# Kernel optimization log

Measured on AMD Instinct MI355X. Metric: run time of the kernel, lower is better.

The kernel has to match this reference:

```python
import jax, jax.numpy as jnp
import numpy as np

DELTA = 1e-7
C = -0.5 * jnp.log(2.0 * jnp.pi)


def _softplus(v):
    return jax.nn.softplus(v) + DELTA


def _log_normal(v, mean=0.0, s=1.0, eps=1e-5):
    return -(v - mean) ** 2 / (2.0 * s ** 2 + eps) - jnp.log(s) + C


def _log_lognormal(v, mean=1.0, s=None, eps=1e-6):
    if s is None:
        s = _softplus(jnp.sqrt(jnp.log(2.0)))  # default prior scale
    return -(jnp.log(v) - mean) ** 2 / (2.0 * s ** 2 + eps) - jnp.log(v) - jnp.log(s) + C


def setup_inputs() -> dict:
    key = jax.random.key(0)
    ks = jax.random.split(key, 14)
    N, K, n_mc = 1024, 2, 64
    inp = {
        'x': jax.random.normal(ks[0], (N, K), dtype=jnp.float32),
        'y': jax.random.normal(ks[1], (N,), dtype=jnp.float32),
        'z': jax.random.normal(ks[2], (n_mc, 5), dtype=jnp.float32),
    }
    names = ['q_beta_m', 'q_beta_s', 'q_sigma2_m', 'q_sigma2_s', 'q_eta_m',
             'q_eta_s', 'q_ls_Z_m', 'q_ls_Z_s', 'q_ls_N_m', 'q_ls_N_s']
    for i, n in enumerate(names):
        inp[n] = jax.random.normal(ks[3 + i], (1,), dtype=jnp.float32)
    return inp


def reference(x, y, z, q_beta_m, q_beta_s, q_sigma2_m, q_sigma2_s,
              q_eta_m, q_eta_s, q_ls_Z_m, q_ls_Z_s, q_ls_N_m, q_ls_N_s):
    N = x.shape[0]
    # reparameterized samples (z plays the role of torch.randn(nMC, 5))
    sigma2 = jnp.exp(z[:, 0] * _softplus(q_sigma2_s) + q_sigma2_m)  # [M]
    beta = z[:, 1] * _softplus(q_beta_s) + q_beta_m                 # [M]
    eta = jnp.exp(z[:, 2] * _softplus(q_eta_s) + q_eta_m)          # [M]
    ls_Z = jnp.exp(z[:, 3] * _softplus(q_ls_Z_s) + q_ls_Z_m)
    ls_N = jnp.exp(z[:, 4] * _softplus(q_ls_N_s) + q_ls_N_m)
    ls = jnp.stack([ls_Z, ls_N], axis=1)                            # [M, 2]

    log_prior = (_log_normal(beta) + _log_lognormal(sigma2) + _log_lognormal(eta)
                 + _log_lognormal(ls[:, 0]) + _log_lognormal(ls[:, 1]))
    log_q = (_log_normal(beta, q_beta_m, _softplus(q_beta_s))
             + _log_lognormal(sigma2, q_sigma2_m, _softplus(q_sigma2_s))
             + _log_lognormal(eta, q_eta_m, _softplus(q_eta_s))
             + _log_lognormal(ls[:, 0], q_ls_Z_m, _softplus(q_ls_Z_s))
             + _log_lognormal(ls[:, 1], q_ls_N_m, _softplus(q_ls_N_s)))

    # RBF covariance per MC sample, built densely (diag of exp(-0.5*0)=1 matches W_ ones diag)
    x_ls = x[None, :, :] / ls[:, None, :]                           # [M, N, K]
    n2 = jnp.sum(x_ls ** 2, axis=-1)                                # [M, N]
    sqd = n2[:, :, None] + n2[:, None, :] - 2.0 * jnp.einsum('mik,mjk->mij', x_ls, x_ls)
    sqd = jnp.maximum(sqd, 0.0)
    cov = eta[:, None, None] * jnp.exp(-0.5 * sqd) + sigma2[:, None, None] * jnp.eye(N, dtype=x.dtype)

    # batched MVN log-prob via Cholesky
    L = jnp.linalg.cholesky(cov)                                    # [M, N, N]
    diff = y[None, :] - beta[:, None]                               # [M, N]
    sol = jax.scipy.linalg.solve_triangular(L, diff[..., None], lower=True)[..., 0]
    quad = jnp.sum(sol ** 2, axis=-1)
    logdet = 2.0 * jnp.sum(jnp.log(jnp.diagonal(L, axis1=-2, axis2=-1)), axis=-1)
    log_L = -0.5 * (quad + logdet + N * jnp.log(2.0 * jnp.pi))

    return log_L + log_prior - log_q
```

## Files before the change

kernel.cpp:

```cpp
#include <hip/hip_runtime.h>
#include <math.h>

#define NN 1024
#define NB 64
#define TB 128
#define CROSS (NN - TB)
#define NSAMP 64
#define SMPL 573440
#define TSQN (TB*TB)
#define PSQN (TB*512)

#define CCONST  (-0.91893853320467274f)
#define LOG2PI  (1.8378770664093453f)

__device__ __forceinline__ int rowoff(int i) {
    int b = i >> 6;
    return (2048*b + 3072)*b + (i & 63)*(64*b + 80);
}
__device__ __forceinline__ float bcastf(float v, int lane) {
    return __int_as_float(__builtin_amdgcn_readlane(__float_as_int(v), lane));
}
__device__ __forceinline__ float softplus_d(float v) {
    return (v > 20.f ? v : log1pf(expf(v))) + 1e-7f;
}
__device__ __forceinline__ float log_normal_f(float v, float mean, float s, float eps) {
    float d = v - mean;
    return -d * d / (2.f * s * s + eps) - logf(s) + CCONST;
}
__device__ __forceinline__ float log_lognormal_f(float v, float mean, float s) {
    float lv = logf(v);
    float d = lv - mean;
    return -d * d / (2.f * s * s + 1e-6f) - lv - logf(s) + CCONST;
}
__device__ __forceinline__ void fma4(float4& c, float a, const float4& b) {
    c.x = fmaf(a, b.x, c.x); c.y = fmaf(a, b.y, c.y);
    c.z = fmaf(a, b.z, c.z); c.w = fmaf(a, b.w, c.w);
}

__global__ void scal_kernel(const float* __restrict__ z,
    const float* qbm, const float* qbs, const float* qsm, const float* qss,
    const float* qem, const float* qes, const float* qzm, const float* qzs,
    const float* qnm, const float* qns, float* __restrict__ scal)
{
    int m = threadIdx.x;
    if (m >= NSAMP) return;
    float z0 = z[m*5+0], z1 = z[m*5+1], z2 = z[m*5+2], z3 = z[m*5+3], z4 = z[m*5+4];
    float spb = softplus_d(qbs[0]);
    float sps = softplus_d(qss[0]);
    float spe = softplus_d(qes[0]);
    float spz = softplus_d(qzs[0]);
    float spn = softplus_d(qns[0]);
    float sigma2 = expf(z0 * sps + qsm[0]);
    float beta   = z1 * spb + qbm[0];
    float eta    = expf(z2 * spe + qem[0]);
    float lsZ    = expf(z3 * spz + qzm[0]);
    float lsN    = expf(z4 * spn + qnm[0]);
    float s0 = softplus_d(sqrtf(logf(2.f)));
    float lp = log_normal_f(beta, 0.f, 1.f, 1e-5f)
             + log_lognormal_f(sigma2, 1.f, s0)
             + log_lognormal_f(eta,    1.f, s0)
             + log_lognormal_f(lsZ,    1.f, s0)
             + log_lognormal_f(lsN,    1.f, s0);
    float lq = log_normal_f(beta, qbm[0], spb, 1e-5f)
             + log_lognormal_f(sigma2, qsm[0], sps)
             + log_lognormal_f(eta,    qem[0], spe)
             + log_lognormal_f(lsZ,    qzm[0], spz)
             + log_lognormal_f(lsN,    qnm[0], spn);
    scal[m]           = sigma2;
    scal[NSAMP + m]   = eta;
    scal[2*NSAMP + m] = 1.f / lsZ;
    scal[3*NSAMP + m] = 1.f / lsN;
    scal[4*NSAMP + m] = beta;
    scal[5*NSAMP + m] = lp - lq;
}

__global__ __launch_bounds__(256)
void covslim_kernel(float* __restrict__ cov, float* __restrict__ tsq,
                    const float* __restrict__ scal,
                    const float* __restrict__ x, const float* __restrict__ y,
                    float* __restrict__ bvec, float* __restrict__ stats, int mbase)
{
    int ml = blockIdx.y;
    int m  = mbase + ml;
    float sigma2 = scal[m];
    float eta    = scal[NSAMP + m];
    float ilZ    = scal[2*NSAMP + m];
    float ilN    = scal[3*NSAMP + m];
    float* C = cov + (size_t)ml * SMPL;
    int tid = threadIdx.x;

    if (blockIdx.x == 0 && tid == 0) { stats[2*m] = 0.f; stats[2*m+1] = 0.f; }

    if (blockIdx.x < 64) {
        int i  = blockIdx.x * 16 + (tid >> 4);
        int j0 = (tid & 15) * 4;
        if ((tid & 15) == 0) bvec[(size_t)m * NN + i] = y[i] - scal[4*NSAMP + m];
        if (j0 > i) return;
        float xi0 = x[2*i]   * ilZ;
        float xi1 = x[2*i+1] * ilN;
        float4 xa = *(const float4*)(x + 2*j0);
        float4 xb = *(const float4*)(x + 2*j0 + 4);
        float v[4]; float d0, d1;
        d0 = xa.x*ilZ - xi0; d1 = xa.y*ilN - xi1; v[0] = eta*__expf(-0.5f*(d0*d0+d1*d1));
        d0 = xa.z*ilZ - xi0; d1 = xa.w*ilN - xi1; v[1] = eta*__expf(-0.5f*(d0*d0+d1*d1));
        d0 = xb.x*ilZ - xi0; d1 = xb.y*ilN - xi1; v[2] = eta*__expf(-0.5f*(d0*d0+d1*d1));
        d0 = xb.z*ilZ - xi0; d1 = xb.w*ilN - xi1; v[3] = eta*__expf(-0.5f*(d0*d0+d1*d1));
        #pragma unroll
        for (int q = 0; q < 4; ++q) if (j0 + q == i) v[q] += sigma2;
        float* row = C + rowoff(i);
        if (j0 + 3 <= i) {
            float4 o; o.x = v[0]; o.y = v[1]; o.z = v[2]; o.w = v[3];
            *(float4*)(row + j0) = o;
        } else {
            #pragma unroll
            for (int q = 0; q < 4; ++q) if (j0 + q <= i) row[j0+q] = v[q];
        }
    } else {
        int bx2 = blockIdx.x - 64;
        int tr  = bx2 * 8 + (tid >> 5);
        int tc  = (tid & 31) * 4;
        int i   = CROSS + tr;
        int j0  = CROSS + tc;
        float xi0 = x[2*i]   * ilZ;
        float xi1 = x[2*i+1] * ilN;
        float4 xa = *(const float4*)(x + 2*j0);
        float4 xb = *(const float4*)(x + 2*j0 + 4);
        float v[4]; float d0, d1;
        d0 = xa.x*ilZ - xi0; d1 = xa.y*ilN - xi1; v[0] = eta*__expf(-0.5f*(d0*d0+d1*d1));
        d0 = xa.z*ilZ - xi0; d1 = xa.w*ilN - xi1; v[1] = eta*__expf(-0.5f*(d0*d0+d1*d1));
        d0 = xb.x*ilZ - xi0; d1 = xb.y*ilN - xi1; v[2] = eta*__expf(-0.5f*(d0*d0+d1*d1));
        d0 = xb.z*ilZ - xi0; d1 = xb.w*ilN - xi1; v[3] = eta*__expf(-0.5f*(d0*d0+d1*d1));
        #pragma unroll
        for (int q = 0; q < 4; ++q) if (j0 + q == i) v[q] += sigma2;
        float4 o; o.x = v[0]; o.y = v[1]; o.z = v[2]; o.w = v[3];
        *(float4*)(tsq + (size_t)ml * TSQN + tr * TB + tc) = o;
    }
}

__global__ __launch_bounds__(256)
void update_kernel(float* __restrict__ covb, const float* __restrict__ scal,
                   const float* __restrict__ x, int mbase, int p, int mc)
{
    int bid = blockIdx.x;
    int ml  = bid % mc;
    int bx  = bid / mc;
    int m  = mbase + ml;
    float* C = covb + (size_t)ml * SMPL;
    int rowbase = p + bx * 128;
    int bofp = rowoff(p);
    int bsp  = 64*(p>>6) + 80;

    __shared__ __align__(16) float As[32][132];
    __shared__ __align__(16) float Bs[32][68];

    int tid = threadIdx.x;
    int tx = tid & 7,  ty = tid >> 3;
    int c0 = tx * 8,   r0 = ty * 4;

    float4 acc[4][2];
    #pragma unroll
    for (int r = 0; r < 4; ++r) { acc[r][0] = make_float4(0,0,0,0); acc[r][1] = make_float4(0,0,0,0); }

    float4 ra[4], rb[2];
    #pragma unroll
    for (int t = 0; t < 4; ++t) {
        int idx = tid + t * 256;
        int ii = idx >> 3, c4 = (idx & 7) << 2;
        int gr = rowbase + ii;
        ra[t] = make_float4(0,0,0,0);
        if (gr < NN) ra[t] = *(const float4*)(C + rowoff(gr) + c4);
    }
    #pragma unroll
    for (int t = 0; t < 2; ++t) {
        int idx = tid + t * 256;
        int ii = idx >> 3, c4 = (idx & 7) << 2;
        rb[t] = *(const float4*)(C + bofp + ii * bsp + c4);
    }

    for (int ks = 0; ks < p; ks += 32) {
        #pragma unroll
        for (int t = 0; t < 4; ++t) {
            int idx = tid + t * 256;
            int ii = idx >> 3, c4 = (idx & 7) << 2;
            As[c4+0][ii] = ra[t].x; As[c4+1][ii] = ra[t].y;
            As[c4+2][ii] = ra[t].z; As[c4+3][ii] = ra[t].w;
        }
        #pragma unroll
        for (int t = 0; t < 2; ++t) {
            int idx = tid + t * 256;
            int ii = idx >> 3, c4 = (idx & 7) << 2;
            Bs[c4+0][ii] = rb[t].x; Bs[c4+1][ii] = rb[t].y;
            Bs[c4+2][ii] = rb[t].z; Bs[c4+3][ii] = rb[t].w;
        }
        __syncthreads();
        int kn = ks + 32;
        if (kn < p) {
            #pragma unroll
            for (int t = 0; t < 4; ++t) {
                int idx = tid + t * 256;
                int ii = idx >> 3, c4 = (idx & 7) << 2;
                int gr = rowbase + ii;
                ra[t] = make_float4(0,0,0,0);
                if (gr < NN) ra[t] = *(const float4*)(C + rowoff(gr) + kn + c4);
            }
            #pragma unroll
            for (int t = 0; t < 2; ++t) {
                int idx = tid + t * 256;
                int ii = idx >> 3, c4 = (idx & 7) << 2;
                rb[t] = *(const float4*)(C + bofp + ii * bsp + kn + c4);
            }
        }
        #pragma unroll
        for (int k = 0; k < 32; ++k) {
            float4 b0 = *(const float4*)&Bs[k][c0];
            float4 b1 = *(const float4*)&Bs[k][c0 + 4];
            float4 a0 = *(const float4*)&As[k][r0];
            float ar[4] = {a0.x, a0.y, a0.z, a0.w};
            #pragma unroll
            for (int r = 0; r < 4; ++r) {
                fma4(acc[r][0], ar[r], b0);
                fma4(acc[r][1], ar[r], b1);
            }
        }
        __syncthreads();
    }

    int jcol = p + c0;
    float sigma2 = scal[m];
    float eta    = scal[NSAMP + m];
    float ilZ    = scal[2*NSAMP + m];
    float ilN    = scal[3*NSAMP + m];
    float4 xa0 = *(const float4*)(x + 2*jcol);
    float4 xb0 = *(const float4*)(x + 2*jcol + 4);
    float4 xa1 = *(const float4*)(x + 2*jcol + 8);
    float4 xb1 = *(const float4*)(x + 2*jcol + 12);
    #pragma unroll
    for (int r = 0; r < 4; ++r) {
        int g = rowbase + r0 + r;
        if (g < NN) {
            float xi0 = x[2*g]   * ilZ;
            float xi1 = x[2*g+1] * ilN;
            float v[8]; float d0, d1;
            d0 = xa0.x*ilZ - xi0; d1 = xa0.y*ilN - xi1; v[0] = eta*__expf(-0.5f*(d0*d0+d1*d1));
            d0 = xa0.z*ilZ - xi0; d1 = xa0.w*ilN - xi1; v[1] = eta*__expf(-0.5f*(d0*d0+d1*d1));
            d0 = xb0.x*ilZ - xi0; d1 = xb0.y*ilN - xi1; v[2] = eta*__expf(-0.5f*(d0*d0+d1*d1));
            d0 = xb0.z*ilZ - xi0; d1 = xb0.w*ilN - xi1; v[3] = eta*__expf(-0.5f*(d0*d0+d1*d1));
            d0 = xa1.x*ilZ - xi0; d1 = xa1.y*ilN - xi1; v[4] = eta*__expf(-0.5f*(d0*d0+d1*d1));
            d0 = xa1.z*ilZ - xi0; d1 = xa1.w*ilN - xi1; v[5] = eta*__expf(-0.5f*(d0*d0+d1*d1));
            d0 = xb1.x*ilZ - xi0; d1 = xb1.y*ilN - xi1; v[6] = eta*__expf(-0.5f*(d0*d0+d1*d1));
            d0 = xb1.z*ilZ - xi0; d1 = xb1.w*ilN - xi1; v[7] = eta*__expf(-0.5f*(d0*d0+d1*d1));
            #pragma unroll
            for (int qq = 0; qq < 8; ++qq) if (jcol + qq == g) v[qq] += sigma2;
            float* cp = C + rowoff(g) + jcol;
            float4 u0, u1;
            u0.x = v[0] - acc[r][0].x; u0.y = v[1] - acc[r][0].y;
            u0.z = v[2] - acc[r][0].z; u0.w = v[3] - acc[r][0].w;
            u1.x = v[4] - acc[r][1].x; u1.y = v[5] - acc[r][1].y;
            u1.z = v[6] - acc[r][1].z; u1.w = v[7] - acc[r][1].w;
            *(float4*)cp = u0;
            *((float4*)cp + 1) = u1;
        }
    }
}

__global__ __launch_bounds__(256)
void update_small_kernel(float* __restrict__ covb, const float* __restrict__ scal,
                         const float* __restrict__ x, int mbase, int p, int mc, int nbx)
{
    int bid  = blockIdx.x;
    int ml   = bid % mc;
    int rest = bid / mc;
    int bx   = rest % nbx;
    int zz   = rest / nbx;
    int m  = mbase + ml;
    float* C = covb + (size_t)ml * SMPL;
    int rowbase = p + bx * 64;
    int zoff = zz * 32;
    int bofp = rowoff(p);
    int bsp  = 64*(p>>6) + 80;

    __shared__ __align__(16) float As[32][68];
    __shared__ __align__(16) float Bs[32][36];

    int tid = threadIdx.x;
    int tx = tid & 7,  ty = tid >> 3;
    int c0 = tx * 4,   r0 = ty * 2;

    float4 acc0 = make_float4(0,0,0,0), acc1 = make_float4(0,0,0,0);

    float4 ra[2], rb1;
    #pragma unroll
    for (int t = 0; t < 2; ++t) {
        int idx = tid + t * 256;
        int ii = idx >> 3, c4 = (idx & 7) << 2;
        int gr = rowbase + ii;
        ra[t] = make_float4(0,0,0,0);
        if (gr < NN) ra[t] = *(const float4*)(C + rowoff(gr) + c4);
    }
    {
        int ii = tid >> 3, c4 = (tid & 7) << 2;
        rb1 = *(const float4*)(C + bofp + (zoff + ii) * bsp + c4);
    }

    for (int ks = 0; ks < p; ks += 32) {
        #pragma unroll
        for (int t = 0; t < 2; ++t) {
            int idx = tid + t * 256;
            int ii = idx >> 3, c4 = (idx & 7) << 2;
            As[c4+0][ii] = ra[t].x; As[c4+1][ii] = ra[t].y;
            As[c4+2][ii] = ra[t].z; As[c4+3][ii] = ra[t].w;
        }
        {
            int ii = tid >> 3, c4 = (tid & 7) << 2;
            Bs[c4+0][ii] = rb1.x; Bs[c4+1][ii] = rb1.y;
            Bs[c4+2][ii] = rb1.z; Bs[c4+3][ii] = rb1.w;
        }
        __syncthreads();
        int kn = ks + 32;
        if (kn < p) {
            #pragma unroll
            for (int t = 0; t < 2; ++t) {
                int idx = tid + t * 256;
                int ii = idx >> 3, c4 = (idx & 7) << 2;
                int gr = rowbase + ii;
                ra[t] = make_float4(0,0,0,0);
                if (gr < NN) ra[t] = *(const float4*)(C + rowoff(gr) + kn + c4);
            }
            {
                int ii = tid >> 3, c4 = (tid & 7) << 2;
                rb1 = *(const float4*)(C + bofp + (zoff + ii) * bsp + kn + c4);
            }
        }
        #pragma unroll
        for (int k = 0; k < 32; ++k) {
            float4 bv = *(const float4*)&Bs[k][c0];
            float2 av = *(const float2*)&As[k][r0];
            fma4(acc0, av.x, bv);
            fma4(acc1, av.y, bv);
        }
        __syncthreads();
    }

    int jcol = p + zoff + c0;
    float sigma2 = scal[m];
    float eta    = scal[NSAMP + m];
    float ilZ    = scal[2*NSAMP + m];
    float ilN    = scal[3*NSAMP + m];
    float4 xa = *(const float4*)(x + 2*jcol);
    float4 xb = *(const float4*)(x + 2*jcol + 4);
    int g0 = rowbase + r0;
    #pragma unroll
    for (int rr = 0; rr < 2; ++rr) {
        int g = g0 + rr;
        if (g < NN) {
            float xi0 = x[2*g]   * ilZ;
            float xi1 = x[2*g+1] * ilN;
            float v[4]; float d0, d1;
            d0 = xa.x*ilZ - xi0; d1 = xa.y*ilN - xi1; v[0] = eta*__expf(-0.5f*(d0*d0+d1*d1));
            d0 = xa.z*ilZ - xi0; d1 = xa.w*ilN - xi1; v[1] = eta*__expf(-0.5f*(d0*d0+d1*d1));
            d0 = xb.x*ilZ - xi0; d1 = xb.y*ilN - xi1; v[2] = eta*__expf(-0.5f*(d0*d0+d1*d1));
            d0 = xb.z*ilZ - xi0; d1 = xb.w*ilN - xi1; v[3] = eta*__expf(-0.5f*(d0*d0+d1*d1));
            #pragma unroll
            for (int qq = 0; qq < 4; ++qq) if (jcol + qq == g) v[qq] += sigma2;
            const float4 ac = (rr == 0) ? acc0 : acc1;
            float* cp = C + rowoff(g) + jcol;
            float4 u;
            u.x = v[0] - ac.x; u.y = v[1] - ac.y; u.z = v[2] - ac.z; u.w = v[3] - ac.w;
            *(float4*)cp = u;
        }
    }
}

__global__ __launch_bounds__(128)
void trsm_kernel(float* __restrict__ covb, float* __restrict__ bvec,
                 float* __restrict__ stats, int mbase, int p, int mc)
{
    int bid = blockIdx.x;
    int ml  = bid % mc;
    int bx  = bid / mc;
    int m  = mbase + ml;
    float* C = covb + (size_t)ml * SMPL;
    __shared__ __align__(16) float Tl[NB][68];
    __shared__ float rs_s[NB], sol_s[NB];
    int tid = threadIdx.x;
    int bofp = rowoff(p);
    int bsp  = 64*(p>>6) + 80;

    int r0 = p + NB + bx * 128 + tid;
    bool have = (r0 < NN);
    float l[NB];
    int roff = have ? rowoff(r0) : 0;
    if (have) {
        const float* rowp = C + roff + p;
        #pragma unroll
        for (int q = 0; q < NB/4; ++q) {
            float4 v = *(const float4*)(rowp + 4*q);
            l[4*q] = v.x; l[4*q+1] = v.y; l[4*q+2] = v.z; l[4*q+3] = v.w;
        }
    }

    if (tid < 64) {
        int r = tid;
        float row[NB];
        const float* src = C + bofp + r * bsp + p;
        #pragma unroll
        for (int q = 0; q < NB/4; ++q) {
            float4 v = *(const float4*)(src + 4*q);
            row[4*q+0] = v.x; row[4*q+1] = v.y; row[4*q+2] = v.z; row[4*q+3] = v.w;
        }
        float b = bvec[(size_t)m * NN + p + r];
        float quad_add = 0.f, my_d = 1.f, my_rs = 0.f, my_sol = 0.f;
        #pragma unroll
        for (int j = 0; j < NB; ++j) {
            float dj = fmaxf(bcastf(row[j], j), 1e-30f);
            float rs = rsqrtf(dj);
            if (r == j) my_d = dj;
            row[j] *= rs;
            float sj = bcastf(b, j) * rs;
            quad_add = fmaf(sj, sj, quad_add);
            b = fmaf(-row[j], sj, b);
            if (r == j) { my_rs = rs; my_sol = sj; }
            #pragma unroll
            for (int c = j + 1; c < NB; ++c) {
                float s = bcastf(row[j], c);
                row[c] = fmaf(-row[j], s, row[c]);
            }
        }
        #pragma unroll
        for (int q = 0; q < NB/4; ++q) {
            float4 v; v.x = row[4*q]; v.y = row[4*q+1]; v.z = row[4*q+2]; v.w = row[4*q+3];
            *(float4*)&Tl[r][4*q] = v;
        }
        rs_s[r]  = my_rs;
        sol_s[r] = my_sol;
        if (bx == 0) {
            float ldv = logf(my_d);
            #pragma unroll
            for (int off = 32; off > 0; off >>= 1) ldv += __shfl_down(ldv, off);
            if (r == 0) {
                stats[2*m]   += quad_add;
                stats[2*m+1] += ldv;
            }
        }
    }
    __syncthreads();

    if (!have) return;
    float* rowp = C + roff + p;
    #pragma unroll
    for (int j = 0; j < NB; ++j) {
        float s0 = l[j], s1 = 0.f, s2 = 0.f, s3 = 0.f;
        int c = 0;
        #pragma unroll
        for (; c + 4 <= j; c += 4) {
            float4 t = *(const float4*)&Tl[j][c];
            s0 = fmaf(-l[c],   t.x, s0);
            s1 = fmaf(-l[c+1], t.y, s1);
            s2 = fmaf(-l[c+2], t.z, s2);
            s3 = fmaf(-l[c+3], t.w, s3);
        }
        #pragma unroll
        for (; c < j; ++c) s0 = fmaf(-l[c], Tl[j][c], s0);
        l[j] = ((s0 + s1) + (s2 + s3)) * rs_s[j];
    }
    #pragma unroll
    for (int q = 0; q < NB/4; ++q) {
        float4 v; v.x = l[4*q]; v.y = l[4*q+1]; v.z = l[4*q+2]; v.w = l[4*q+3];
        *(float4*)(rowp + 4*q) = v;
    }
    float b0 = 0.f, b1 = 0.f, b2 = 0.f, b3 = 0.f;
    #pragma unroll
    for (int j = 0; j < NB; j += 4) {
        b0 = fmaf(l[j],   sol_s[j],   b0);
        b1 = fmaf(l[j+1], sol_s[j+1], b1);
        b2 = fmaf(l[j+2], sol_s[j+2], b2);
        b3 = fmaf(l[j+3], sol_s[j+3], b3);
    }
    bvec[(size_t)m * NN + r0] -= ((b0 + b1) + (b2 + b3));
}

__global__ __launch_bounds__(256)
void tailsyrk_kernel(const float* __restrict__ covb, float* __restrict__ psq)
{
    int ml = blockIdx.y;
    const float* C = covb + (size_t)ml * SMPL;
    float* P = psq + (size_t)ml * PSQN;
    int z  = blockIdx.x;
    int k0 = z * (CROSS / 4);

    __shared__ __align__(16) float As[32][132];
    int tid = threadIdx.x;
    int tx = tid & 15, ty = tid >> 4;
    int c0 = tx * 8, r0 = ty * 8;

    float4 acc[8][2];
    #pragma unroll
    for (int r = 0; r < 8; ++r) { acc[r][0] = make_float4(0,0,0,0); acc[r][1] = make_float4(0,0,0,0); }

    for (int ks = k0; ks < k0 + CROSS/4; ks += 32) {
        for (int idx = tid; idx < 128 * 8; idx += 256) {
            int ii = idx >> 3;
            int c4 = (idx & 7) << 2;
            float4 v = *(const float4*)(C + rowoff(CROSS + ii) + ks + c4);
            As[c4+0][ii] = v.x; As[c4+1][ii] = v.y;
            As[c4+2][ii] = v.z; As[c4+3][ii] = v.w;
        }
        __syncthreads();
        #pragma unroll
        for (int k = 0; k < 32; ++k) {
            float4 b0 = *(const float4*)&As[k][c0];
            float4 b1 = *(const float4*)&As[k][c0 + 4];
            float4 a0 = *(const float4*)&As[k][r0];
            float4 a1 = *(const float4*)&As[k][r0 + 4];
            float ar[8] = {a0.x, a0.y, a0.z, a0.w, a1.x, a1.y, a1.z, a1.w};
            #pragma unroll
            for (int r = 0; r < 8; ++r) {
                fma4(acc[r][0], ar[r], b0);
                fma4(acc[r][1], ar[r], b1);
            }
        }
        __syncthreads();
    }

    #pragma unroll
    for (int r = 0; r < 8; ++r) {
        float* cp = P + (r0 + r) * 512 + z * 128 + c0;
        *(float4*)cp = acc[r][0];
        *((float4*)cp + 1) = acc[r][1];
    }
}

__global__ __launch_bounds__(512)
void finish_kernel(const float* __restrict__ tsq, const float* __restrict__ psq,
                   const float* __restrict__ bvec,
                   const float* __restrict__ stats, float* __restrict__ out,
                   const float* __restrict__ scal, int mbase)
{
    int ml = blockIdx.x;
    int m  = mbase + ml;
    const float* T = tsq + (size_t)ml * TSQN;
    const float* P = psq + (size_t)ml * PSQN;
    __shared__ __align__(16) float A11[NB][68];
    __shared__ __align__(16) float A21[NB][68];
    __shared__ __align__(16) float A22[NB][68];
    __shared__ float rs_s[NB], sol_s[NB];
    __shared__ float bt[TB];
    __shared__ float s_quad, s_ld;
    int tid = threadIdx.x;

    if (tid < TB) bt[tid] = bvec[(size_t)m * NN + CROSS + tid];
    if (tid == 0) { s_quad = 0.f; s_ld = 0.f; }

    float4 tv[6], p0[6], p1[6], p2[6], p3[6];
    const float* pbase[6];
    #pragma unroll
    for (int u = 0; u < 6; ++u) {
        int f   = tid + u * 512;
        int i   = (f & 1023) >> 4;
        int c4  = (f & 15) << 2;
        int blk = f >> 10;
        int ti  = (blk == 0) ? i : (64 + i);
        int tc  = (blk == 2) ? (64 + c4) : c4;
        pbase[u] = P + ti * 512 + tc;
        tv[u] = *(const float4*)(T + ti * TB + tc);
    }
    #pragma unroll
    for (int u = 0; u < 6; ++u) p0[u] = *(const float4*)(pbase[u]);
    #pragma unroll
    for (int u = 0; u < 6; ++u) p1[u] = *(const float4*)(pbase[u] + 128);
    #pragma unroll
    for (int u = 0; u < 6; ++u) p2[u] = *(const float4*)(pbase[u] + 256);
    #pragma unroll
    for (int u = 0; u < 6; ++u) p3[u] = *(const float4*)(pbase[u] + 384);
    #pragma unroll
    for (int u = 0; u < 6; ++u) {
        int f   = tid + u * 512;
        int i   = (f & 1023) >> 4;
        int c4  = (f & 15) << 2;
        int blk = f >> 10;
        float4 s;
        s.x = ((p0[u].x + p1[u].x) + p2[u].x) + p3[u].x;
        s.y = ((p0[u].y + p1[u].y) + p2[u].y) + p3[u].y;
        s.z = ((p0[u].z + p1[u].z) + p2[u].z) + p3[u].z;
        s.w = ((p0[u].w + p1[u].w) + p2[u].w) + p3[u].w;
        float4 t = tv[u];
        t.x -= s.x; t.y -= s.y; t.z -= s.z; t.w -= s.w;
        float* dst = (blk == 0) ? &A11[i][c4] : ((blk == 1) ? &A21[i][c4] : &A22[i][c4]);
        *(float4*)dst = t;
    }
    __syncthreads();

    if (tid < 64) {
        int r = tid;
        float row[NB];
        #pragma unroll
        for (int q = 0; q < NB/4; ++q) {
            float4 v = *(const float4*)&A11[r][4*q];
            row[4*q+0] = v.x; row[4*q+1] = v.y; row[4*q+2] = v.z; row[4*q+3] = v.w;
        }
        float b = bt[r];
        float quad_add = 0.f, my_d = 1.f;
        #pragma unroll
        for (int j = 0; j < NB; ++j) {
            float dj = fmaxf(bcastf(row[j], j), 1e-30f);
            float rs = rsqrtf(dj);
            if (r == j) my_d = dj;
            row[j] *= rs;
            float sj = bcastf(b, j) * rs;
            quad_add = fmaf(sj, sj, quad_add);
            b = fmaf(-row[j], sj, b);
            if (r == j) { rs_s[j] = rs; sol_s[j] = sj; }
            #pragma unroll
            for (int c = j + 1; c < NB; ++c) {
                float s = bcastf(row[j], c);
                row[c] = fmaf(-row[j], s, row[c]);
            }
        }
        #pragma unroll
        for (int q = 0; q < NB/4; ++q) {
            float4 v; v.x = row[4*q]; v.y = row[4*q+1]; v.z = row[4*q+2]; v.w = row[4*q+3];
            *(float4*)&A11[r][4*q] = v;
        }
        float ldv = logf(my_d);
        #pragma unroll
        for (int off = 32; off > 0; off >>= 1) ldv += __shfl_down(ldv, off);
        if (r == 0) { s_quad += quad_add; s_ld += ldv; }
    }
    __syncthreads();

    if (tid >= 64 && tid < 128) {
        int rr = tid - 64;
        float l[NB];
        #pragma unroll
        for (int q = 0; q < NB/4; ++q) {
            float4 v = *(const float4*)&A21[rr][4*q];
            l[4*q] = v.x; l[4*q+1] = v.y; l[4*q+2] = v.z; l[4*q+3] = v.w;
        }
        #pragma unroll
        for (int j = 0; j < NB; ++j) {
            float s0 = l[j], s1 = 0.f, s2 = 0.f, s3 = 0.f;
            int c = 0;
            #pragma unroll
            for (; c + 4 <= j; c += 4) {
                float4 t = *(const float4*)&A11[j][c];
                s0 = fmaf(-l[c],   t.x, s0);
                s1 = fmaf(-l[c+1], t.y, s1);
                s2 = fmaf(-l[c+2], t.z, s2);
                s3 = fmaf(-l[c+3], t.w, s3);
            }
            #pragma unroll
            for (; c < j; ++c) s0 = fmaf(-l[c], A11[j][c], s0);
            l[j] = ((s0 + s1) + (s2 + s3)) * rs_s[j];
        }
        #pragma unroll
        for (int k = 0; k < NB; ++k) A11[k][rr] = l[k];
        float bacc = 0.f;
        #pragma unroll
        for (int j = 0; j < NB; ++j) bacc = fmaf(l[j], sol_s[j], bacc);
        bt[64 + rr] -= bacc;
    }
    __syncthreads();

    for (int idx = tid; idx < 64 * 16; idx += 512) {
        int i  = idx >> 4;
        int j4 = (idx & 15) << 2;
        if (j4 > i) continue;
        float4 a = make_float4(0,0,0,0);
        #pragma unroll 8
        for (int k = 0; k < NB; ++k) {
            float4 pj = *(const float4*)&A11[k][j4];
            fma4(a, A11[k][i], pj);
        }
        float* cp = &A22[i][j4];
        float4 uu = *(float4*)cp;
        uu.x -= a.x; uu.y -= a.y; uu.z -= a.z; uu.w -= a.w;
        *(float4*)cp = uu;
    }
    __syncthreads();

    if (tid < 64) {
        int r = tid;
        float row[NB];
        #pragma unroll
        for (int q = 0; q < NB/4; ++q) {
            float4 v = *(const float4*)&A22[r][4*q];
            row[4*q+0] = v.x; row[4*q+1] = v.y; row[4*q+2] = v.z; row[4*q+3] = v.w;
        }
        float b = bt[64 + r];
        float quad_add = 0.f, my_d = 1.f;
        #pragma unroll
        for (int j = 0; j < NB; ++j) {
            float dj = fmaxf(bcastf(row[j], j), 1e-30f);
            float rs = rsqrtf(dj);
            if (r == j) my_d = dj;
            row[j] *= rs;
            float sj = bcastf(b, j) * rs;
            quad_add = fmaf(sj, sj, quad_add);
            b = fmaf(-row[j], sj, b);
            #pragma unroll
            for (int c = j + 1; c < NB; ++c) {
                float s = bcastf(row[j], c);
                row[c] = fmaf(-row[j], s, row[c]);
            }
        }
        float ldv = logf(my_d);
        #pragma unroll
        for (int off = 32; off > 0; off >>= 1) ldv += __shfl_down(ldv, off);
        if (r == 0) { s_quad += quad_add; s_ld += ldv; }
    }
    __syncthreads();

    if (tid == 0) {
        float qt = stats[2*m]   + s_quad;
        float lt = stats[2*m+1] + s_ld;
        out[m] = -0.5f * (qt + lt + (float)NN * LOG2PI) + scal[5*NSAMP + m];
    }
}

extern "C" void kernel_launch(void* const* d_in, const int* in_sizes, int n_in,
                              void* d_out, int out_size, void* d_ws, size_t ws_size,
                              hipStream_t stream)
{
    const float* x   = (const float*)d_in[0];
    const float* y   = (const float*)d_in[1];
    const float* z   = (const float*)d_in[2];
    const float* qbm = (const float*)d_in[3];
    const float* qbs = (const float*)d_in[4];
    const float* qsm = (const float*)d_in[5];
    const float* qss = (const float*)d_in[6];
    const float* qem = (const float*)d_in[7];
    const float* qes = (const float*)d_in[8];
    const float* qzm = (const float*)d_in[9];
    const float* qzs = (const float*)d_in[10];
    const float* qnm = (const float*)d_in[11];
    const float* qns = (const float*)d_in[12];
    float* out  = (float*)d_out;
    float* ws   = (float*)d_ws;

    float* scal   = ws;
    float* bvec   = ws + 1024;
    float* stats  = ws + 1024 + NSAMP*NN;
    float* tsq    = ws + 1024 + NSAMP*NN + 512;
    float* psq    = tsq + (size_t)NSAMP * TSQN;
    float* cov    = psq + (size_t)NSAMP * PSQN;
    size_t headF  = 1024 + (size_t)NSAMP*NN + 512;

    scal_kernel<<<1, 64, 0, stream>>>(z, qbm, qbs, qsm, qss, qem, qes, qzm, qzs, qnm, qns, scal);

    size_t availF = ws_size / 4;
    size_t perM   = (size_t)SMPL + TSQN + PSQN;
    int mc_max = NSAMP;
    if (availF < headF + (size_t)NSAMP * perM) {
        size_t rem = (availF > headF) ? (availF - headF) : 0;
        mc_max = (int)(rem / perM);
        if (mc_max < 1) mc_max = 1;
        if (mc_max > NSAMP) mc_max = NSAMP;
    }

    for (int mb = 0; mb < NSAMP; mb += mc_max) {
        int mc = NSAMP - mb; if (mc > mc_max) mc = mc_max;
        covslim_kernel<<<dim3(80, mc), 256, 0, stream>>>(cov, tsq, scal, x, y, bvec, stats, mb);
        for (int q = 0; q < CROSS / NB; ++q) {
            int p = q * NB;
            if (q > 0) {
                int rows = NN - p;
                int rt128 = (rows + 127) / 128;
                if (rt128 * mc >= 448) {
                    update_kernel<<<dim3(rt128 * mc), 256, 0, stream>>>(cov, scal, x, mb, p, mc);
                } else {
                    int rt64 = (rows + 63) / 64;
                    update_small_kernel<<<dim3(rt64 * mc * 2), 256, 0, stream>>>(cov, scal, x, mb, p, mc, rt64);
                }
            }
            int rb = NN - p - NB;
            int rtiles = (rb + 127) / 128;
            trsm_kernel<<<dim3(rtiles * mc), 128, 0, stream>>>(cov, bvec, stats, mb, p, mc);
        }
        tailsyrk_kernel<<<dim3(4, mc), 256, 0, stream>>>(cov, psq);
        finish_kernel<<<mc, 512, 0, stream>>>(tsq, psq, bvec, stats, out, scal, mb);
    }
}
```

Baseline: 1.157 ms.

## Drop split-K partials in tail SYRK, prefetch tiles, subtract into tsq directly

The tail SYRK no longer splits K across 4 blocks that write partial products to a psq buffer. A single block per sample now loops over the full K range, register-prefetches the next 32-wide tile while computing the current one, and subtracts its result from tsq in place. The finish kernel stops reading and summing the four partials, and covslim switches to a 1D grid with the sample index interleaved. This removes the psq workspace and its traffic but cuts tail-SYRK parallelism from 4*mc to mc blocks, giving each block a four-times-longer serial K loop.

```diff
diff --git a/kernel.cpp b/kernel.cpp
--- a/kernel.cpp
+++ b/kernel.cpp
@@ -8,7 +8,6 @@
 #define NSAMP 64
 #define SMPL 573440
 #define TSQN (TB*TB)
-#define PSQN (TB*512)
 
 #define CCONST  (-0.91893853320467274f)
 #define LOG2PI  (1.8378770664093453f)
@@ -78,9 +77,12 @@
 void covslim_kernel(float* __restrict__ cov, float* __restrict__ tsq,
                     const float* __restrict__ scal,
                     const float* __restrict__ x, const float* __restrict__ y,
-                    float* __restrict__ bvec, float* __restrict__ stats, int mbase)
+                    float* __restrict__ bvec, float* __restrict__ stats,
+                    int mbase, int mc)
 {
-    int ml = blockIdx.y;
+    int bid = blockIdx.x;
+    int ml  = bid % mc;
+    int bx  = bid / mc;
     int m  = mbase + ml;
     float sigma2 = scal[m];
     float eta    = scal[NSAMP + m];
@@ -89,10 +91,10 @@
     float* C = cov + (size_t)ml * SMPL;
     int tid = threadIdx.x;
 
-    if (blockIdx.x == 0 && tid == 0) { stats[2*m] = 0.f; stats[2*m+1] = 0.f; }
-
-    if (blockIdx.x < 64) {
-        int i  = blockIdx.x * 16 + (tid >> 4);
+    if (bx == 0 && tid == 0) { stats[2*m] = 0.f; stats[2*m+1] = 0.f; }
+
+    if (bx < 64) {
+        int i  = bx * 16 + (tid >> 4);
         int j0 = (tid & 15) * 4;
         if ((tid & 15) == 0) bvec[(size_t)m * NN + i] = y[i] - scal[4*NSAMP + m];
         if (j0 > i) return;
@@ -116,7 +118,7 @@
             for (int q = 0; q < 4; ++q) if (j0 + q <= i) row[j0+q] = v[q];
         }
     } else {
-        int bx2 = blockIdx.x - 64;
+        int bx2 = bx - 64;
         int tr  = bx2 * 8 + (tid >> 5);
         int tc  = (tid & 31) * 4;
         int i   = CROSS + tr;
@@ -480,13 +482,11 @@
 }
 
 __global__ __launch_bounds__(256)
-void tailsyrk_kernel(const float* __restrict__ covb, float* __restrict__ psq)
+void tailsyrk_kernel(const float* __restrict__ covb, float* __restrict__ tsq)
 {
-    int ml = blockIdx.y;
+    int ml = blockIdx.x;
     const float* C = covb + (size_t)ml * SMPL;
-    float* P = psq + (size_t)ml * PSQN;
-    int z  = blockIdx.x;
-    int k0 = z * (CROSS / 4);
+    float* T = tsq + (size_t)ml * TSQN;
 
     __shared__ __align__(16) float As[32][132];
     int tid = threadIdx.x;
@@ -497,15 +497,32 @@
     #pragma unroll
     for (int r = 0; r < 8; ++r) { acc[r][0] = make_float4(0,0,0,0); acc[r][1] = make_float4(0,0,0,0); }
 
-    for (int ks = k0; ks < k0 + CROSS/4; ks += 32) {
-        for (int idx = tid; idx < 128 * 8; idx += 256) {
-            int ii = idx >> 3;
-            int c4 = (idx & 7) << 2;
-            float4 v = *(const float4*)(C + rowoff(CROSS + ii) + ks + c4);
-            As[c4+0][ii] = v.x; As[c4+1][ii] = v.y;
-            As[c4+2][ii] = v.z; As[c4+3][ii] = v.w;
+    float4 ra[4];
+    #pragma unroll
+    for (int t = 0; t < 4; ++t) {
+        int idx = tid + t * 256;
+        int ii = idx >> 3, c4 = (idx & 7) << 2;
+        ra[t] = *(const float4*)(C + rowoff(CROSS + ii) + c4);
+    }
+
+    for (int ks = 0; ks < CROSS; ks += 32) {
+        #pragma unroll
+        for (int t = 0; t < 4; ++t) {
+            int idx = tid + t * 256;
+            int ii = idx >> 3, c4 = (idx & 7) << 2;
+            As[c4+0][ii] = ra[t].x; As[c4+1][ii] = ra[t].y;
+            As[c4+2][ii] = ra[t].z; As[c4+3][ii] = ra[t].w;
         }
         __syncthreads();
+        int kn = ks + 32;
+        if (kn < CROSS) {
+            #pragma unroll
+            for (int t = 0; t < 4; ++t) {
+                int idx = tid + t * 256;
+                int ii = idx >> 3, c4 = (idx & 7) << 2;
+                ra[t] = *(const float4*)(C + rowoff(CROSS + ii) + kn + c4);
+            }
+        }
         #pragma unroll
         for (int k = 0; k < 32; ++k) {
             float4 b0 = *(const float4*)&As[k][c0];
@@ -524,22 +541,24 @@
 
     #pragma unroll
     for (int r = 0; r < 8; ++r) {
-        float* cp = P + (r0 + r) * 512 + z * 128 + c0;
-        *(float4*)cp = acc[r][0];
-        *((float4*)cp + 1) = acc[r][1];
+        float* cp = T + (r0 + r) * TB + c0;
+        float4 u0 = *(float4*)cp;
+        float4 u1 = *((float4*)cp + 1);
+        u0.x -= acc[r][0].x; u0.y -= acc[r][0].y; u0.z -= acc[r][0].z; u0.w -= acc[r][0].w;
+        u1.x -= acc[r][1].x; u1.y -= acc[r][1].y; u1.z -= acc[r][1].z; u1.w -= acc[r][1].w;
+        *(float4*)cp = u0;
+        *((float4*)cp + 1) = u1;
     }
 }
 
 __global__ __launch_bounds__(512)
-void finish_kernel(const float* __restrict__ tsq, const float* __restrict__ psq,
-                   const float* __restrict__ bvec,
+void finish_kernel(const float* __restrict__ tsq, const float* __restrict__ bvec,
                    const float* __restrict__ stats, float* __restrict__ out,
                    const float* __restrict__ scal, int mbase)
 {
     int ml = blockIdx.x;
     int m  = mbase + ml;
     const float* T = tsq + (size_t)ml * TSQN;
-    const float* P = psq + (size_t)ml * PSQN;
     __shared__ __align__(16) float A11[NB][68];
     __shared__ __align__(16) float A21[NB][68];
     __shared__ __align__(16) float A22[NB][68];
@@ -551,8 +570,6 @@
     if (tid < TB) bt[tid] = bvec[(size_t)m * NN + CROSS + tid];
     if (tid == 0) { s_quad = 0.f; s_ld = 0.f; }
 
-    float4 tv[6], p0[6], p1[6], p2[6], p3[6];
-    const float* pbase[6];
     #pragma unroll
     for (int u = 0; u < 6; ++u) {
         int f   = tid + u * 512;
@@ -561,30 +578,7 @@
         int blk = f >> 10;
         int ti  = (blk == 0) ? i : (64 + i);
         int tc  = (blk == 2) ? (64 + c4) : c4;
-        pbase[u] = P + ti * 512 + tc;
-        tv[u] = *(const float4*)(T + ti * TB + tc);
-    }
-    #pragma unroll
-    for (int u = 0; u < 6; ++u) p0[u] = *(const float4*)(pbase[u]);
-    #pragma unroll
-    for (int u = 0; u < 6; ++u) p1[u] = *(const float4*)(pbase[u] + 128);
-    #pragma unroll
-    for (int u = 0; u < 6; ++u) p2[u] = *(const float4*)(pbase[u] + 256);
-    #pragma unroll
-    for (int u = 0; u < 6; ++u) p3[u] = *(const float4*)(pbase[u] + 384);
-    #pragma unroll
-    for (int u = 0; u < 6; ++u) {
-        int f   = tid + u * 512;
-        int i   = (f & 1023) >> 4;
-        int c4  = (f & 15) << 2;
-        int blk = f >> 10;
-        float4 s;
-        s.x = ((p0[u].x + p1[u].x) + p2[u].x) + p3[u].x;
-        s.y = ((p0[u].y + p1[u].y) + p2[u].y) + p3[u].y;
-        s.z = ((p0[u].z + p1[u].z) + p2[u].z) + p3[u].z;
-        s.w = ((p0[u].w + p1[u].w) + p2[u].w) + p3[u].w;
-        float4 t = tv[u];
-        t.x -= s.x; t.y -= s.y; t.z -= s.z; t.w -= s.w;
+        float4 t = *(const float4*)(T + ti * TB + tc);
         float* dst = (blk == 0) ? &A11[i][c4] : ((blk == 1) ? &A21[i][c4] : &A22[i][c4]);
         *(float4*)dst = t;
     }
@@ -741,14 +735,13 @@
     float* bvec   = ws + 1024;
     float* stats  = ws + 1024 + NSAMP*NN;
     float* tsq    = ws + 1024 + NSAMP*NN + 512;
-    float* psq    = tsq + (size_t)NSAMP * TSQN;
-    float* cov    = psq + (size_t)NSAMP * PSQN;
+    float* cov    = tsq + (size_t)NSAMP * TSQN;
     size_t headF  = 1024 + (size_t)NSAMP*NN + 512;
 
     scal_kernel<<<1, 64, 0, stream>>>(z, qbm, qbs, qsm, qss, qem, qes, qzm, qzs, qnm, qns, scal);
 
     size_t availF = ws_size / 4;
-    size_t perM   = (size_t)SMPL + TSQN + PSQN;
+    size_t perM   = (size_t)SMPL + TSQN;
     int mc_max = NSAMP;
     if (availF < headF + (size_t)NSAMP * perM) {
         size_t rem = (availF > headF) ? (availF - headF) : 0;
@@ -759,7 +752,7 @@
 
     for (int mb = 0; mb < NSAMP; mb += mc_max) {
         int mc = NSAMP - mb; if (mc > mc_max) mc = mc_max;
-        covslim_kernel<<<dim3(80, mc), 256, 0, stream>>>(cov, tsq, scal, x, y, bvec, stats, mb);
+        covslim_kernel<<<dim3(80 * mc), 256, 0, stream>>>(cov, tsq, scal, x, y, bvec, stats, mb, mc);
         for (int q = 0; q < CROSS / NB; ++q) {
             int p = q * NB;
             if (q > 0) {
@@ -776,7 +769,7 @@
             int rtiles = (rb + 127) / 128;
             trsm_kernel<<<dim3(rtiles * mc), 128, 0, stream>>>(cov, bvec, stats, mb, p, mc);
         }
-        tailsyrk_kernel<<<dim3(4, mc), 256, 0, stream>>>(cov, psq);
-        finish_kernel<<<mc, 512, 0, stream>>>(tsq, psq, bvec, stats, out, scal, mb);
-    }
-}
+        tailsyrk_kernel<<<dim3(mc), 256, 0, stream>>>(cov, tsq);
+        finish_kernel<<<mc, 512, 0, stream>>>(tsq, bvec, stats, out, scal, mb);
+    }
+}
```

After: 2.357 ms. 104% more time.
